# Optimization experiments

Hardware: AMD Instinct MI355X
Metric: run time of the kernel (lower is better)

## Reference

```python
import jax, jax.numpy as jnp
import numpy as np

NUM_CLASSES = 15
ANGLE_BINS = 90
ANGLE_SCALE = float(np.pi / 2 / ANGLE_BINS)
TOPK, A_ALPHA, A_BETA = 13, 1.0, 6.0
F_ALPHA, F_GAMMA = 0.75, 2.0
W_CLS, W_BOX, W_ANGLE = 1.0, 2.5, 0.05
EPS = 1e-9


def make_anchors(img=1024, strides=(8, 16, 32)):
    pts, strs = [], []
    for s in strides:
        n = img // s
        xs = (np.arange(n, dtype=np.float32) + 0.5) * s  # pixel-space centers
        X, Y = np.meshgrid(xs, xs)
        pts.append(np.stack([X.ravel(), Y.ravel()], -1))
        strs.append(np.full((n * n, 1), s, np.float32))
    return np.concatenate(pts)[None].astype(np.float32), np.concatenate(strs)[None]


def decode_boxes(anchor_points, reg_dist, raw_angles, stride_tensor, angle_proj):
    # DFL-style angle: softmax over bins projected onto angle values
    angle = jnp.einsum('bna,a->bn', jax.nn.softmax(raw_angles, axis=-1), angle_proj)  # [B,N]
    lt, rb = reg_dist[..., :2], reg_dist[..., 2:]
    off = (rb - lt) * 0.5
    c, s = jnp.cos(angle), jnp.sin(angle)
    ox = off[..., 0] * c - off[..., 1] * s
    oy = off[..., 0] * s + off[..., 1] * c
    xy = jnp.stack([ox, oy], -1) * stride_tensor + anchor_points
    wh = (lt + rb) * stride_tensor
    return jnp.concatenate([xy, wh, angle[..., None]], -1)  # [B,N,5]


def _cov(b):
    # rotated box -> 2D Gaussian covariance terms
    w, h, a = b[..., 2], b[..., 3], b[..., 4]
    A, B = w * w / 12.0, h * h / 12.0
    c, s = jnp.cos(a), jnp.sin(a)
    return A * c * c + B * s * s, A * s * s + B * c * c, (A - B) * c * s


def probiou_hd(b1, b2, eps=1e-3):
    # Hellinger distance between Gaussian boxes; probiou similarity = 1 - hd
    x1, y1, x2, y2 = b1[..., 0], b1[..., 1], b2[..., 0], b2[..., 1]
    a1, bb1, c1 = _cov(b1)
    a2, bb2, c2 = _cov(b2)
    denom = (a1 + a2) * (bb1 + bb2) - (c1 + c2) ** 2 + eps
    t1 = ((a1 + a2) * (y1 - y2) ** 2 + (bb1 + bb2) * (x1 - x2) ** 2) / denom * 0.25
    t2 = ((c1 + c2) * (x2 - x1) * (y1 - y2)) / denom * 0.5
    det1 = jnp.maximum(a1 * bb1 - c1 * c1, 0.0)
    det2 = jnp.maximum(a2 * bb2 - c2 * c2, 0.0)
    t3 = 0.5 * jnp.log(denom / (4.0 * jnp.sqrt(det1 * det2) + eps) + eps)
    bd = jnp.clip(t1 + t2 + t3, eps, 100.0)
    return jnp.sqrt(1.0 - jnp.exp(-bd) + 1e-7)


def assign(pred_scores, pred_boxes, anchor_points, gt_labels, gt_boxes, pad_gt_mask, bg_index):
    B, M = gt_labels.shape[:2]
    N = pred_boxes.shape[1]
    C = pred_scores.shape[-1]
    lbl = gt_labels[..., 0]  # [B,M]
    # rotated ProbIoU between every GT and every pred box: [B,M,N]
    ious = jnp.maximum(1.0 - probiou_hd(gt_boxes[:, :, None, :], pred_boxes[:, None, :, :]), 0.0)
    # gather pred class score at each gt's label: [B,M,N]
    scores = jnp.einsum('bnc,bmc->bmn', pred_scores, jax.nn.one_hot(lbl, C, dtype=pred_scores.dtype))
    align = (scores ** A_ALPHA) * (ious ** A_BETA)
    # anchor-center inside rotated GT box
    dx = anchor_points[:, None, :, 0] - gt_boxes[:, :, None, 0]
    dy = anchor_points[:, None, :, 1] - gt_boxes[:, :, None, 1]
    ca, sa = jnp.cos(gt_boxes[:, :, None, 4]), jnp.sin(gt_boxes[:, :, None, 4])
    xr = dx * ca + dy * sa
    yr = -dx * sa + dy * ca
    in_gt = (jnp.abs(xr) < gt_boxes[:, :, None, 2] * 0.5) & (jnp.abs(yr) < gt_boxes[:, :, None, 3] * 0.5)
    mask_cand = in_gt.astype(align.dtype) * pad_gt_mask  # [B,M,N]
    # top-k alignment candidates per GT
    topv, topi = jax.lax.top_k(align * mask_cand, TOPK)
    valid = (topv > EPS).astype(align.dtype)
    bi = jnp.arange(B)[:, None, None]
    mi = jnp.arange(M)[None, :, None]
    topk_mask = jnp.zeros((B, M, N), align.dtype).at[bi, mi, topi].max(valid)
    mask_pos = topk_mask * mask_cand
    # resolve anchors matched to multiple GTs via max IoU
    fg = mask_pos.sum(1)  # [B,N]
    is_max_iou = jax.nn.one_hot(jnp.argmax(ious, axis=1), M, axis=1, dtype=align.dtype)
    mask_pos = jnp.where(fg[:, None, :] > 1, is_max_iou, mask_pos)
    fg = mask_pos.sum(1)
    tgt_idx = jnp.argmax(mask_pos, axis=1)  # [B,N]
    fg_mask = fg > 0
    assigned_labels = jnp.where(fg_mask, jnp.take_along_axis(lbl, tgt_idx, axis=1), bg_index)
    assigned_boxes = jnp.take_along_axis(gt_boxes, tgt_idx[..., None], axis=1)  # [B,N,5]
    # normalize alignment metric by per-GT max IoU / max align
    align_pos = align * mask_pos
    max_align = align_pos.max(-1, keepdims=True)
    max_iou = (ious * mask_pos).max(-1, keepdims=True)
    norm_align = (align_pos * max_iou / (max_align + EPS)).max(1)  # [B,N]
    onehot = jax.nn.one_hot(assigned_labels, C + 1, dtype=align.dtype)[..., :C]
    assigned_scores = onehot * norm_align[..., None]
    return assigned_labels, assigned_boxes, assigned_scores


def _bce_logits(x, t):
    return jnp.maximum(x, 0.0) - x * t + jnp.log1p(jnp.exp(-jnp.abs(x)))


def compute_loss(cls_logits, reg_dist, raw_angles, gt_labels, gt_boxes, valid_mask,
                 anchor_points, stride_tensor, angle_proj):
    C = NUM_CLASSES
    decoded = decode_boxes(anchor_points, reg_dist, raw_angles, stride_tensor, angle_proj)
    cls_scores = jax.nn.sigmoid(cls_logits)
    al, ab, ascore = assign(jax.lax.stop_gradient(cls_scores), jax.lax.stop_gradient(decoded),
                            anchor_points, gt_labels, gt_boxes, valid_mask, C)
    score_sum = jnp.maximum(ascore.sum(), 1.0)
    # varifocal classification loss
    onehot = jax.nn.one_hot(al, C + 1, dtype=cls_logits.dtype)[..., :C]
    fw = F_ALPHA * (cls_scores ** F_GAMMA) * (1.0 - onehot) + ascore * onehot
    loss_cls = (_bce_logits(cls_logits, ascore) * fw).sum() / score_sum
    # ProbIoU box loss over positives, weighted by assigned scores
    posf = (al != C).astype(cls_logits.dtype)
    iou_loss = probiou_hd(decoded, ab)  # [B,N]
    bw = ascore.sum(-1)
    loss_box = (iou_loss * bw * posf).sum() / score_sum
    # DFL angle loss: interpolate CE between neighboring bins
    t = jnp.clip(ab[..., 4] / ANGLE_SCALE, 0.0, ANGLE_BINS - 0.01)
    li = t.astype(jnp.int32)
    ri = jnp.minimum(li + 1, ANGLE_BINS)
    lw = ri.astype(t.dtype) - t
    rw = 1.0 - lw
    logp = jax.nn.log_softmax(raw_angles, axis=-1)
    ce_l = -jnp.take_along_axis(logp, li[..., None], axis=-1)[..., 0]
    ce_r = -jnp.take_along_axis(logp, ri[..., None], axis=-1)[..., 0]
    npos = jnp.maximum(posf.sum(), 1.0)
    loss_angle = ((ce_l * lw + ce_r * rw) * posf).sum() / npos
    total = W_CLS * loss_cls + W_BOX * loss_box + W_ANGLE * loss_angle
    return total, loss_cls, loss_box, loss_angle


def setup_inputs() -> dict:
    key = jax.random.key(0)
    ks = jax.random.split(key, 8)
    B, M, C, AB = 16, 64, NUM_CLASSES, ANGLE_BINS
    anchor_np, stride_np = make_anchors()
    N = anchor_np.shape[1]  # 21504
    cls_logits = jax.random.normal(ks[0], (B, N, C), jnp.float32) - 2.0
    reg_dist = jax.random.uniform(ks[1], (B, N, 4), jnp.float32, 0.0, 6.0)
    raw_angles = jax.random.normal(ks[2], (B, N, AB + 1), jnp.float32)
    gt_labels = jax.random.randint(ks[3], (B, M, 1), 0, C)
    cxy = jax.random.uniform(ks[4], (B, M, 2), jnp.float32, 32.0, 992.0)
    wh = jax.random.uniform(ks[5], (B, M, 2), jnp.float32, 16.0, 160.0)
    ang = jax.random.uniform(ks[6], (B, M, 1), jnp.float32, 0.0, float(np.pi / 2) - 1e-3)
    gt_boxes = jnp.concatenate([cxy, wh, ang], -1)
    valid_mask = (jax.random.uniform(ks[7], (B, M, 1)) < 0.8).astype(jnp.float32)
    angle_proj = jnp.arange(AB + 1, dtype=jnp.float32) * ANGLE_SCALE
    return dict(cls_logits=cls_logits, reg_dist=reg_dist, raw_angles=raw_angles,
                gt_labels=gt_labels, gt_boxes=gt_boxes, valid_mask=valid_mask,
                anchor_points=jnp.asarray(anchor_np), stride_tensor=jnp.asarray(stride_np),
                angle_proj=angle_proj)


def reference(cls_logits, reg_dist, raw_angles, gt_labels, gt_boxes, valid_mask,
              anchor_points, stride_tensor, angle_proj):
    return compute_loss(cls_logits, reg_dist, raw_angles, gt_labels, gt_boxes, valid_mask,
                        anchor_points, stride_tensor, angle_proj)
```

## Files before the change

### kernel.cpp

```cpp
#include <hip/hip_runtime.h>

#define TK 13
#define EPSA 1e-9f
#define MMAX 128
#define CMAX 1024
#define DROWS 64
#define A1F 91
#define CF 15

__device__ __forceinline__ float frcp(float x) { return __builtin_amdgcn_rcpf(x); }

__device__ __forceinline__ void anchor_of(int n, float& ax, float& ay, float& st) {
    if (n < 16384)      { st = 8.0f;  ax = ((n & 127) + 0.5f) * 8.0f;  ay = ((n >> 7) + 0.5f) * 8.0f; }
    else if (n < 20480) { int q = n - 16384; st = 16.0f; ax = ((q & 63) + 0.5f) * 16.0f; ay = ((q >> 6) + 0.5f) * 16.0f; }
    else                { int q = n - 20480; st = 32.0f; ax = ((q & 31) + 0.5f) * 32.0f; ay = ((q >> 5) + 0.5f) * 32.0f; }
}

__device__ __forceinline__ float hd_cov(float x1, float y1, float a1, float b1, float c1, float sd1,
                                        float x2, float y2, float a2, float b2, float c2, float sd2) {
    float sa = a1 + a2, sb = b1 + b2, sc = c1 + c2;
    float denom = sa * sb - sc * sc + 1e-3f;
    float inv = frcp(denom);
    float dy = y1 - y2, dx = x1 - x2;
    float t1 = (sa * dy * dy + sb * dx * dx) * inv * 0.25f;
    float t2 = sc * (x2 - x1) * (y1 - y2) * inv * 0.5f;
    float t3 = 0.5f * __logf(denom * frcp(4.0f * sd1 * sd2 + 1e-3f) + 1e-3f);
    float bd = fminf(fmaxf(t1 + t2 + t3, 1e-3f), 100.0f);
    return sqrtf(1.0f - __expf(-bd) + 1e-7f);
}

__device__ __forceinline__ void cov5(float w, float h, float ang,
                                     float& ca, float& cb, float& cc, float& sd) {
    float A = w * w * (1.0f / 12.0f), B = h * h * (1.0f / 12.0f);
    float c = __cosf(ang), s = __sinf(ang);
    ca = A * c * c + B * s * s;
    cb = A * s * s + B * c * c;
    cc = (A - B) * c * s;
    sd = sqrtf(fmaxf(ca * cb - cc * cc, 0.0f));
}

__global__ __launch_bounds__(256) void k_decode(
    const float* __restrict__ reg, const float* __restrict__ rawang,
    float* __restrict__ dec6, float* __restrict__ lse_out,
    int* __restrict__ zbase, int zwords,
    int BN, int N) {
    __shared__ float srow[DROWS * A1F];
    int tid = threadIdx.x;
    int gidx = blockIdx.x * 256 + tid;
    if (gidx < zwords) zbase[gidx] = 0;
    int r0 = blockIdx.x * DROWS;
    if (r0 >= BN) return;
    if (r0 + DROWS <= BN) {
        const float4* g4 = (const float4*)(rawang + (size_t)r0 * A1F);
        float4* s4 = (float4*)srow;
#pragma unroll
        for (int k = 0; k < (DROWS * A1F) / 4 / 256 + 1; ++k) {
            int j = tid + k * 256;
            if (j < (DROWS * A1F) / 4) s4[j] = g4[j];
        }
    } else {
        const float* gs = rawang + (size_t)r0 * A1F;
        int lim = (BN - r0) * A1F;
        for (int k = tid; k < lim; k += 256) srow[k] = gs[k];
    }
    __syncthreads();
    int row = tid >> 2, sub = tid & 3;
    int idx = r0 + row;
    if (idx >= BN) return;
    int j0 = sub * 23;
    int jn = (sub == 3) ? 22 : 23;
    const float* rp = srow + row * A1F + j0;
    float s = 0.0f, num = 0.0f;
#pragma unroll
    for (int i = 0; i < 23; ++i) {
        if (i < jn) {
            float e = __expf(rp[i]);
            s += e;
            num = fmaf(e, (float)(j0 + i), num);
        }
    }
    s += __shfl_xor(s, 1); num += __shfl_xor(num, 1);
    s += __shfl_xor(s, 2); num += __shfl_xor(num, 2);
    if (sub == 0) {
        float ang = 0.017453292519943295f * num * frcp(s);
        float lse = __logf(s);
        int n = idx % N;
        float4 rg = *(const float4*)(reg + (size_t)idx * 4);
        float l0 = rg.x, l1 = rg.y, rr0 = rg.z, rr1 = rg.w;
        float offx = (rr0 - l0) * 0.5f, offy = (rr1 - l1) * 0.5f;
        float c = __cosf(ang), sn = __sinf(ang);
        float ox = offx * c - offy * sn, oy = offx * sn + offy * c;
        float ax, ay, st;
        anchor_of(n, ax, ay, st);
        float x = ox * st + ax;
        float y = oy * st + ay;
        float w = (l0 + rr0) * st, hh = (l1 + rr1) * st;
        float ca, cb, cc, sd;
        cov5(w, hh, ang, ca, cb, cc, sd);
        float* d = dec6 + (size_t)idx * 6;
        d[0] = x; d[1] = y; d[2] = ca; d[3] = cb; d[4] = cc; d[5] = sd;
        lse_out[idx] = lse;
    }
}

__global__ __launch_bounds__(256) void k_topk(
    const float* __restrict__ dec6, const float* __restrict__ cls,
    const float* __restrict__ gtb, const int* __restrict__ gtl,
    const float* __restrict__ vmask,
    int* __restrict__ fg, int* __restrict__ tgtc,
    int B, int M, int N, int C) {
    int m = blockIdx.x, b = blockIdx.y;
    if (vmask[b * M + m] == 0.0f) return;
    const float* g = gtb + (size_t)(b * M + m) * 5;
    float gx = g[0], gy = g[1], gw = g[2], gh = g[3], gang = g[4];
    float gca, gcb, gcc, gsd;
    cov5(gw, gh, gang, gca, gcb, gcc, gsd);
    float cA = __cosf(gang), sA = __sinf(gang);
    int lbl = gtl[b * M + m];
    float hw = 0.5f * gw, hh2 = 0.5f * gh;
    float hx = fabsf(hw * cA) + fabsf(hh2 * sA);
    float hy = fabsf(hw * sA) + fabsf(hh2 * cA);
    int tid = threadIdx.x;
    size_t bN = (size_t)b * N;

    __shared__ int cnt;
    __shared__ float cval[CMAX];
    __shared__ int cidx[CMAX];
    if (tid == 0) cnt = 0;
    __syncthreads();

    const int off_[3] = {0, 16384, 20480};
    const int gs_[3]  = {128, 64, 32};
    const float st_[3] = {8.0f, 16.0f, 32.0f};
#pragma unroll
    for (int lv = 0; lv < 3; ++lv) {
        float st = st_[lv];
        int gs = gs_[lv], off = off_[lv];
        float ist = frcp(st);
        int i0 = (int)floorf((gx - hx) * ist - 0.5f);
        int i1 = (int)ceilf((gx + hx) * ist - 0.5f);
        int j0 = (int)floorf((gy - hy) * ist - 0.5f);
        int j1 = (int)ceilf((gy + hy) * ist - 0.5f);
        i0 = max(i0, 0); j0 = max(j0, 0);
        i1 = min(i1, gs - 1); j1 = min(j1, gs - 1);
        int w = i1 - i0 + 1, hgt = j1 - j0 + 1;
        int tot = (w > 0 && hgt > 0) ? w * hgt : 0;
        for (int t = tid; t < tot; t += 256) {
            int ii = i0 + t % w, jj = j0 + t / w;
            float ax = (ii + 0.5f) * st, ay = (jj + 0.5f) * st;
            float dx = ax - gx, dy = ay - gy;
            float xr = dx * cA + dy * sA;
            float yr = -dx * sA + dy * cA;
            if (fabsf(xr) < hw && fabsf(yr) < hh2) {
                int n = off + jj * gs + ii;
                const float* d = dec6 + (bN + n) * 6;
                float hd = hd_cov(gx, gy, gca, gcb, gcc, gsd,
                                  d[0], d[1], d[2], d[3], d[4], d[5]);
                float iou = fmaxf(1.0f - hd, 0.0f);
                float xl = cls[(bN + n) * C + lbl];
                float p = frcp(1.0f + __expf(-xl));
                float i2 = iou * iou;
                float v = p * (i2 * i2 * i2);
                if (v > EPSA) {
                    int pos = atomicAdd(&cnt, 1);
                    if (pos < CMAX) { cval[pos] = v; cidx[pos] = n; }
                }
            }
        }
    }
    __syncthreads();

    int total = min(cnt, CMAX);
    int rounds = min(total, TK);
    if (tid < 64) {
        for (int r = 0; r < rounds; ++r) {
            float bv = -1.0f; int bn = 0x7fffffff; int bp = -1;
            for (int j = tid; j < total; j += 64) {
                float v = cval[j];
                int nn = cidx[j];
                if (v > bv || (v == bv && nn < bn)) { bv = v; bn = nn; bp = j; }
            }
            for (int o = 32; o; o >>= 1) {
                float ov = __shfl_xor(bv, o);
                int on = __shfl_xor(bn, o);
                int op = __shfl_xor(bp, o);
                if (ov > bv || (ov == bv && on < bn)) { bv = ov; bn = on; bp = op; }
            }
            if (tid == 0) {
                atomicAdd(&fg[bN + bn], 1);
                atomicMax(&tgtc[bN + bn], m);
            }
            if ((bp & 63) == tid) cval[bp] = -2.0f;
        }
    }
}

__global__ __launch_bounds__(256) void k_select(
    const float* __restrict__ dec6, const float* __restrict__ cls,
    const float* __restrict__ gtb, const int* __restrict__ gtl,
    const int* __restrict__ fg, const int* __restrict__ tgtc,
    int* __restrict__ tgt_out, float* __restrict__ align_out,
    unsigned int* __restrict__ max_align, unsigned int* __restrict__ max_iou,
    int B, int M, int N, int C) {
    __shared__ float gx[MMAX], gy[MMAX], ga[MMAX], gb[MMAX], gc[MMAX], gsd[MMAX];
    __shared__ int glb[MMAX];
    int b = blockIdx.y;
    int tid = threadIdx.x;
    if (tid < M) {
        const float* g = gtb + (size_t)(b * M + tid) * 5;
        float ca, cb, cc, sd;
        cov5(g[2], g[3], g[4], ca, cb, cc, sd);
        gx[tid] = g[0]; gy[tid] = g[1]; ga[tid] = ca; gb[tid] = cb; gc[tid] = cc; gsd[tid] = sd;
        glb[tid] = gtl[b * M + tid];
    }
    __syncthreads();
    int n = blockIdx.x * 256 + tid;
    if (n >= N) return;
    size_t bN = (size_t)b * N;
    int f = fg[bN + n];
    if (f == 0) {
        tgt_out[bN + n] = -1;
        align_out[bN + n] = 0.0f;
        return;
    }
    const float* d = dec6 + (bN + n) * 6;
    float px = d[0], py = d[1], pa = d[2], pb = d[3], pc = d[4], psd = d[5];
    int mstar;
    float ioustar;
    if (f == 1) {
        mstar = tgtc[bN + n];
        float hd = hd_cov(gx[mstar], gy[mstar], ga[mstar], gb[mstar], gc[mstar], gsd[mstar],
                          px, py, pa, pb, pc, psd);
        ioustar = fmaxf(1.0f - hd, 0.0f);
    } else {
        float best = -1.0f; int bm = 0;
        for (int mm = 0; mm < M; mm++) {
            float hd = hd_cov(gx[mm], gy[mm], ga[mm], gb[mm], gc[mm], gsd[mm],
                              px, py, pa, pb, pc, psd);
            float iou = fmaxf(1.0f - hd, 0.0f);
            if (iou > best) { best = iou; bm = mm; }
        }
        mstar = bm; ioustar = best;
    }
    int lbl = glb[mstar];
    float xl = cls[(bN + n) * C + lbl];
    float p = frcp(1.0f + __expf(-xl));
    float i2 = ioustar * ioustar;
    float al = p * (i2 * i2 * i2);
    tgt_out[bN + n] = mstar;
    align_out[bN + n] = al;
    atomicMax(&max_align[b * M + mstar], __float_as_uint(al));
    atomicMax(&max_iou[b * M + mstar], __float_as_uint(ioustar));
}

__global__ __launch_bounds__(256) void k_loss(
    const float* __restrict__ dec6, const float* __restrict__ cls,
    const float* __restrict__ rawang, const float* __restrict__ lse_in,
    const float* __restrict__ gtb, const int* __restrict__ gtl,
    const int* __restrict__ tgt_in, const float* __restrict__ align_in,
    const float* __restrict__ max_align, const float* __restrict__ max_iou,
    float* __restrict__ pblk, int* __restrict__ ticket, float* __restrict__ out,
    int B, int M, int N, int C, int A1, int nblk) {
    __shared__ float gx[MMAX], gy[MMAX], ga[MMAX], gb[MMAX], gc[MMAX], gsd[MMAX], gan[MMAX];
    __shared__ int glb[MMAX];
    int b = blockIdx.y;
    int tid = threadIdx.x;
    if (tid < M) {
        const float* g = gtb + (size_t)(b * M + tid) * 5;
        float ca, cb, cc, sd;
        cov5(g[2], g[3], g[4], ca, cb, cc, sd);
        gx[tid] = g[0]; gy[tid] = g[1]; ga[tid] = ca; gb[tid] = cb; gc[tid] = cc; gsd[tid] = sd;
        gan[tid] = g[4];
        glb[tid] = gtl[b * M + tid];
    }
    __syncthreads();
    int n = blockIdx.x * 256 + tid;
    float s_cls = 0.0f, s_box = 0.0f, s_ang = 0.0f, s_asc = 0.0f, s_pos = 0.0f;
    if (n < N) {
        size_t bN = (size_t)b * N;
        int tg = tgt_in[bN + n];
        int lbl = -1;
        float norm = 0.0f;
        if (tg >= 0) {
            lbl = glb[tg];
            norm = align_in[bN + n] * max_iou[b * M + tg] * frcp(max_align[b * M + tg] + 1e-9f);
            const float* d = dec6 + (bN + n) * 6;
            float hd = hd_cov(d[0], d[1], d[2], d[3], d[4], d[5],
                              gx[tg], gy[tg], ga[tg], gb[tg], gc[tg], gsd[tg]);
            s_box = hd * norm;
            s_asc = norm;
            s_pos = 1.0f;
            float tt = fminf(fmaxf(gan[tg] * 57.29577951308232f, 0.0f), 89.99f);
            int li = (int)tt;
            int ri = min(li + 1, 90);
            float lw = (float)ri - tt;
            float rw = 1.0f - lw;
            float lse = lse_in[bN + n];
            const float* arow = rawang + (bN + n) * A1;
            float ce_l = lse - arow[li];
            float ce_r = lse - arow[ri];
            s_ang = ce_l * lw + ce_r * rw;
        }
        const float* xrow = cls + (bN + n) * CF;
#pragma unroll
        for (int c = 0; c < CF; c++) {
            float x = xrow[c];
            float e = __expf(-fabsf(x));
            float inv = frcp(1.0f + e);
            float p = (x >= 0.0f) ? inv : 1.0f - inv;
            bool pos = (c == lbl);
            float t = pos ? norm : 0.0f;
            float fw = pos ? norm : 0.75f * p * p;
            float bce = fmaxf(x, 0.0f) - x * t - __logf(inv);
            s_cls += bce * fw;
        }
    }
    for (int off = 32; off; off >>= 1) {
        s_cls += __shfl_xor(s_cls, off);
        s_box += __shfl_xor(s_box, off);
        s_ang += __shfl_xor(s_ang, off);
        s_asc += __shfl_xor(s_asc, off);
        s_pos += __shfl_xor(s_pos, off);
    }
    __shared__ float red[4][5];
    __shared__ int slast;
    int w = tid >> 6, lane = tid & 63;
    if (lane == 0) {
        red[w][0] = s_cls; red[w][1] = s_box; red[w][2] = s_ang;
        red[w][3] = s_asc; red[w][4] = s_pos;
    }
    __syncthreads();
    if (tid == 0) {
        int bid = blockIdx.y * gridDim.x + blockIdx.x;
        float* p = pblk + (size_t)bid * 5;
        p[0] = red[0][0] + red[1][0] + red[2][0] + red[3][0];
        p[1] = red[0][1] + red[1][1] + red[2][1] + red[3][1];
        p[2] = red[0][2] + red[1][2] + red[2][2] + red[3][2];
        p[3] = red[0][3] + red[1][3] + red[2][3] + red[3][3];
        p[4] = red[0][4] + red[1][4] + red[2][4] + red[3][4];
        __threadfence();
        int t = atomicAdd(ticket, 1);
        slast = (t == nblk - 1) ? 1 : 0;
    }
    __syncthreads();
    if (!slast) return;
    float a0 = 0, a1 = 0, a2 = 0, a3 = 0, a4 = 0;
    for (int j = tid; j < nblk; j += 256) {
        const float* p = pblk + (size_t)j * 5;
        a0 += p[0]; a1 += p[1]; a2 += p[2]; a3 += p[3]; a4 += p[4];
    }
    for (int off = 32; off; off >>= 1) {
        a0 += __shfl_xor(a0, off);
        a1 += __shfl_xor(a1, off);
        a2 += __shfl_xor(a2, off);
        a3 += __shfl_xor(a3, off);
        a4 += __shfl_xor(a4, off);
    }
    if (lane == 0) { red[w][0] = a0; red[w][1] = a1; red[w][2] = a2; red[w][3] = a3; red[w][4] = a4; }
    __syncthreads();
    if (tid == 0) {
        float s0 = 0, s1 = 0, s2 = 0, s3 = 0, s4 = 0;
        for (int i = 0; i < 4; i++) {
            s0 += red[i][0]; s1 += red[i][1]; s2 += red[i][2]; s3 += red[i][3]; s4 += red[i][4];
        }
        float ssum = fmaxf(s3, 1.0f);
        float npos = fmaxf(s4, 1.0f);
        float lc = s0 / ssum;
        float lb = s1 / ssum;
        float la = s2 / npos;
        out[0] = 1.0f * lc + 2.5f * lb + 0.05f * la;
        out[1] = lc;
        out[2] = lb;
        out[3] = la;
    }
}

extern "C" void kernel_launch(void* const* d_in, const int* in_sizes, int n_in,
                              void* d_out, int out_size, void* d_ws, size_t ws_size,
                              hipStream_t stream) {
    const float* cls    = (const float*)d_in[0];
    const float* reg    = (const float*)d_in[1];
    const float* rawang = (const float*)d_in[2];
    const int*   gtl    = (const int*)d_in[3];
    const float* gtb    = (const float*)d_in[4];
    const float* vmask  = (const float*)d_in[5];

    int N  = in_sizes[6] / 2;
    int B  = in_sizes[1] / (4 * N);
    int BN = B * N;
    int C  = in_sizes[0] / BN;
    int M  = in_sizes[3] / B;
    int A1 = in_sizes[2] / BN;

    float* ws = (float*)d_ws;
    float* dec6     = ws;
    float* lse      = dec6 + (size_t)BN * 6;
    float* align_at = lse + BN;
    int*   tgt      = (int*)(align_at + BN);
    int*   fg       = tgt + BN;
    int*   tgtc     = fg + BN;
    unsigned int* mxal = (unsigned int*)(tgtc + BN);
    unsigned int* mxio = mxal + B * M;
    int*   ticket   = (int*)(mxio + B * M);
    float* pblk     = (float*)(ticket + 4);

    int zwords = BN * 2 + B * M * 2 + 4;

    k_decode<<<dim3((BN + DROWS - 1) / DROWS), dim3(256), 0, stream>>>(
        reg, rawang, dec6, lse, fg, zwords, BN, N);
    k_topk<<<dim3(M, B), dim3(256), 0, stream>>>(
        dec6, cls, gtb, gtl, vmask, fg, tgtc, B, M, N, C);
    int gx = (N + 255) / 256;
    dim3 g45(gx, B);
    k_select<<<g45, dim3(256), 0, stream>>>(
        dec6, cls, gtb, gtl, fg, tgtc, tgt, align_at, mxal, mxio, B, M, N, C);
    k_loss<<<g45, dim3(256), 0, stream>>>(
        dec6, cls, rawang, lse, gtb, gtl, tgt, align_at,
        (const float*)mxal, (const float*)mxio, pblk, ticket, (float*)d_out,
        B, M, N, C, A1, gx * B);
}
```

Measured before the change: 317.7 us.

## Split decoded boxes into float4+float2 arrays, zero targets in decode, add final-reduce kernel

The 6-float decoded record is stored as separate float4 and float2 arrays so each gather becomes two vector loads instead of six scalar loads. The target and alignment arrays are now zeroed in the decode kernel through a grid-stride loop, and target indices are stored as m+1. This lets k_select skip writing for unassigned anchors. The last-block ticket reduction in k_loss is replaced by a separate single-block k_final kernel, trading the atomic and fence for an extra launch.

```diff
diff --git a/kernel.cpp b/kernel.cpp
--- a/kernel.cpp
+++ b/kernel.cpp
@@ -41,13 +41,14 @@
 
 __global__ __launch_bounds__(256) void k_decode(
     const float* __restrict__ reg, const float* __restrict__ rawang,
-    float* __restrict__ dec6, float* __restrict__ lse_out,
+    float4* __restrict__ dec4, float2* __restrict__ dcs,
+    float* __restrict__ lse_out,
     int* __restrict__ zbase, int zwords,
     int BN, int N) {
     __shared__ float srow[DROWS * A1F];
     int tid = threadIdx.x;
-    int gidx = blockIdx.x * 256 + tid;
-    if (gidx < zwords) zbase[gidx] = 0;
+    int gstride = gridDim.x * 256;
+    for (int z = blockIdx.x * 256 + tid; z < zwords; z += gstride) zbase[z] = 0;
     int r0 = blockIdx.x * DROWS;
     if (r0 >= BN) return;
     if (r0 + DROWS <= BN) {
@@ -97,14 +98,15 @@
         float w = (l0 + rr0) * st, hh = (l1 + rr1) * st;
         float ca, cb, cc, sd;
         cov5(w, hh, ang, ca, cb, cc, sd);
-        float* d = dec6 + (size_t)idx * 6;
-        d[0] = x; d[1] = y; d[2] = ca; d[3] = cb; d[4] = cc; d[5] = sd;
+        dec4[idx] = make_float4(x, y, ca, cb);
+        dcs[idx] = make_float2(cc, sd);
         lse_out[idx] = lse;
     }
 }
 
 __global__ __launch_bounds__(256) void k_topk(
-    const float* __restrict__ dec6, const float* __restrict__ cls,
+    const float4* __restrict__ dec4, const float2* __restrict__ dcs,
+    const float* __restrict__ cls,
     const float* __restrict__ gtb, const int* __restrict__ gtl,
     const float* __restrict__ vmask,
     int* __restrict__ fg, int* __restrict__ tgtc,
@@ -153,9 +155,10 @@
             float yr = -dx * sA + dy * cA;
             if (fabsf(xr) < hw && fabsf(yr) < hh2) {
                 int n = off + jj * gs + ii;
-                const float* d = dec6 + (bN + n) * 6;
+                float4 dd = dec4[bN + n];
+                float2 cs = dcs[bN + n];
                 float hd = hd_cov(gx, gy, gca, gcb, gcc, gsd,
-                                  d[0], d[1], d[2], d[3], d[4], d[5]);
+                                  dd.x, dd.y, dd.z, dd.w, cs.x, cs.y);
                 float iou = fmaxf(1.0f - hd, 0.0f);
                 float xl = cls[(bN + n) * C + lbl];
                 float p = frcp(1.0f + __expf(-xl));
@@ -196,7 +199,8 @@
 }
 
 __global__ __launch_bounds__(256) void k_select(
-    const float* __restrict__ dec6, const float* __restrict__ cls,
+    const float4* __restrict__ dec4, const float2* __restrict__ dcs,
+    const float* __restrict__ cls,
     const float* __restrict__ gtb, const int* __restrict__ gtl,
     const int* __restrict__ fg, const int* __restrict__ tgtc,
     int* __restrict__ tgt_out, float* __restrict__ align_out,
@@ -218,13 +222,10 @@
     if (n >= N) return;
     size_t bN = (size_t)b * N;
     int f = fg[bN + n];
-    if (f == 0) {
-        tgt_out[bN + n] = -1;
-        align_out[bN + n] = 0.0f;
-        return;
-    }
-    const float* d = dec6 + (bN + n) * 6;
-    float px = d[0], py = d[1], pa = d[2], pb = d[3], pc = d[4], psd = d[5];
+    if (f == 0) return;
+    float4 dd = dec4[bN + n];
+    float2 cs = dcs[bN + n];
+    float px = dd.x, py = dd.y, pa = dd.z, pb = dd.w, pc = cs.x, psd = cs.y;
     int mstar;
     float ioustar;
     if (f == 1) {
@@ -247,20 +248,21 @@
     float p = frcp(1.0f + __expf(-xl));
     float i2 = ioustar * ioustar;
     float al = p * (i2 * i2 * i2);
-    tgt_out[bN + n] = mstar;
+    tgt_out[bN + n] = mstar + 1;
     align_out[bN + n] = al;
     atomicMax(&max_align[b * M + mstar], __float_as_uint(al));
     atomicMax(&max_iou[b * M + mstar], __float_as_uint(ioustar));
 }
 
 __global__ __launch_bounds__(256) void k_loss(
-    const float* __restrict__ dec6, const float* __restrict__ cls,
+    const float4* __restrict__ dec4, const float2* __restrict__ dcs,
+    const float* __restrict__ cls,
     const float* __restrict__ rawang, const float* __restrict__ lse_in,
     const float* __restrict__ gtb, const int* __restrict__ gtl,
     const int* __restrict__ tgt_in, const float* __restrict__ align_in,
     const float* __restrict__ max_align, const float* __restrict__ max_iou,
-    float* __restrict__ pblk, int* __restrict__ ticket, float* __restrict__ out,
-    int B, int M, int N, int C, int A1, int nblk) {
+    float* __restrict__ pblk,
+    int B, int M, int N, int C, int A1) {
     __shared__ float gx[MMAX], gy[MMAX], ga[MMAX], gb[MMAX], gc[MMAX], gsd[MMAX], gan[MMAX];
     __shared__ int glb[MMAX];
     int b = blockIdx.y;
@@ -278,14 +280,16 @@
     float s_cls = 0.0f, s_box = 0.0f, s_ang = 0.0f, s_asc = 0.0f, s_pos = 0.0f;
     if (n < N) {
         size_t bN = (size_t)b * N;
-        int tg = tgt_in[bN + n];
+        int tg1 = tgt_in[bN + n];
         int lbl = -1;
         float norm = 0.0f;
-        if (tg >= 0) {
+        if (tg1 > 0) {
+            int tg = tg1 - 1;
             lbl = glb[tg];
             norm = align_in[bN + n] * max_iou[b * M + tg] * frcp(max_align[b * M + tg] + 1e-9f);
-            const float* d = dec6 + (bN + n) * 6;
-            float hd = hd_cov(d[0], d[1], d[2], d[3], d[4], d[5],
+            float4 dd = dec4[bN + n];
+            float2 cs = dcs[bN + n];
+            float hd = hd_cov(dd.x, dd.y, dd.z, dd.w, cs.x, cs.y,
                               gx[tg], gy[tg], ga[tg], gb[tg], gc[tg], gsd[tg]);
             s_box = hd * norm;
             s_asc = norm;
@@ -323,7 +327,6 @@
         s_pos += __shfl_xor(s_pos, off);
     }
     __shared__ float red[4][5];
-    __shared__ int slast;
     int w = tid >> 6, lane = tid & 63;
     if (lane == 0) {
         red[w][0] = s_cls; red[w][1] = s_box; red[w][2] = s_ang;
@@ -338,12 +341,12 @@
         p[2] = red[0][2] + red[1][2] + red[2][2] + red[3][2];
         p[3] = red[0][3] + red[1][3] + red[2][3] + red[3][3];
         p[4] = red[0][4] + red[1][4] + red[2][4] + red[3][4];
-        __threadfence();
-        int t = atomicAdd(ticket, 1);
-        slast = (t == nblk - 1) ? 1 : 0;
-    }
-    __syncthreads();
-    if (!slast) return;
+    }
+}
+
+__global__ __launch_bounds__(256) void k_final(
+    const float* __restrict__ pblk, int nblk, float* __restrict__ out) {
+    int tid = threadIdx.x;
     float a0 = 0, a1 = 0, a2 = 0, a3 = 0, a4 = 0;
     for (int j = tid; j < nblk; j += 256) {
         const float* p = pblk + (size_t)j * 5;
@@ -356,6 +359,8 @@
         a3 += __shfl_xor(a3, off);
         a4 += __shfl_xor(a4, off);
     }
+    __shared__ float red[4][5];
+    int w = tid >> 6, lane = tid & 63;
     if (lane == 0) { red[w][0] = a0; red[w][1] = a1; red[w][2] = a2; red[w][3] = a3; red[w][4] = a4; }
     __syncthreads();
     if (tid == 0) {
@@ -393,29 +398,29 @@
     int A1 = in_sizes[2] / BN;
 
     float* ws = (float*)d_ws;
-    float* dec6     = ws;
-    float* lse      = dec6 + (size_t)BN * 6;
-    float* align_at = lse + BN;
-    int*   tgt      = (int*)(align_at + BN);
-    int*   fg       = tgt + BN;
-    int*   tgtc     = fg + BN;
-    unsigned int* mxal = (unsigned int*)(tgtc + BN);
+    float4* dec4    = (float4*)ws;
+    float2* dcs     = (float2*)(dec4 + BN);
+    float*  lse     = (float*)(dcs + BN);
+    int*    fg      = (int*)(lse + BN);
+    int*    tgtc    = fg + BN;
+    int*    tgt     = tgtc + BN;
+    float*  align_at = (float*)(tgt + BN);
+    unsigned int* mxal = (unsigned int*)(align_at + BN);
     unsigned int* mxio = mxal + B * M;
-    int*   ticket   = (int*)(mxio + B * M);
-    float* pblk     = (float*)(ticket + 4);
-
-    int zwords = BN * 2 + B * M * 2 + 4;
+    float*  pblk    = (float*)(mxio + B * M);
+
+    int zwords = BN * 4 + B * M * 2;
 
     k_decode<<<dim3((BN + DROWS - 1) / DROWS), dim3(256), 0, stream>>>(
-        reg, rawang, dec6, lse, fg, zwords, BN, N);
+        reg, rawang, dec4, dcs, lse, fg, zwords, BN, N);
     k_topk<<<dim3(M, B), dim3(256), 0, stream>>>(
-        dec6, cls, gtb, gtl, vmask, fg, tgtc, B, M, N, C);
+        dec4, dcs, cls, gtb, gtl, vmask, fg, tgtc, B, M, N, C);
     int gx = (N + 255) / 256;
     dim3 g45(gx, B);
     k_select<<<g45, dim3(256), 0, stream>>>(
-        dec6, cls, gtb, gtl, fg, tgtc, tgt, align_at, mxal, mxio, B, M, N, C);
+        dec4, dcs, cls, gtb, gtl, fg, tgtc, tgt, align_at, mxal, mxio, B, M, N, C);
     k_loss<<<g45, dim3(256), 0, stream>>>(
-        dec6, cls, rawang, lse, gtb, gtl, tgt, align_at,
-        (const float*)mxal, (const float*)mxio, pblk, ticket, (float*)d_out,
-        B, M, N, C, A1, gx * B);
-}
+        dec4, dcs, cls, rawang, lse, gtb, gtl, tgt, align_at,
+        (const float*)mxal, (const float*)mxio, pblk, B, M, N, C, A1);
+    k_final<<<1, 256, 0, stream>>>(pblk, gx * B, (float*)d_out);
+}
```

After: 295.9 us. 1.07x faster.
